# Performance work log

Hardware: AMD Instinct MI355X
Metric: run time of the kernel (lower is better)

The kernel has to match this reference:

```python
import jax, jax.numpy as jnp
import numpy as np

B, N, D = 8, 4096, 512
H, R = 8, 256
DEPTH = D // H


def setup_inputs() -> dict:
    key = jax.random.key(0)
    ks = jax.random.split(key, 8)
    g = lambda k, shape, fan: jax.random.normal(k, shape, jnp.float32) * np.sqrt(2.0 / fan)
    return {
        "x": jax.random.normal(ks[0], (B, N, D), jnp.float32),
        "wq": g(ks[1], (D, D), 2 * D),
        "wk": g(ks[2], (D, D), 2 * D),
        "wv": g(ks[3], (D, D), 2 * D),
        "E": g(ks[4], (H, N, R), N + R),
        "F": g(ks[5], (H, N, R), N + R),
        "w_dense": g(ks[6], (D, D), 2 * D),
        "b_dense": jnp.zeros((D,), jnp.float32),
    }


def reference(x, wq, wk, wv, E, F, w_dense, b_dense):
    b = x.shape[0]
    split = lambda t: t.reshape(b, N, H, DEPTH).transpose(0, 2, 1, 3)  # -> bhnd
    q = split(x @ wq)
    k = split(x @ wk)
    v = split(x @ wv)
    # low-rank Linformer projections of K and V along sequence dim
    k_proj = jnp.einsum('bhnd,hnr->bhrd', k, E)
    v_proj = jnp.einsum('bhnd,hnr->bhrd', v, F)
    scores = jnp.einsum('bhnd,bhrd->bhnr', q, k_proj) / jnp.sqrt(jnp.float32(DEPTH))
    attn = jax.nn.softmax(scores, axis=-1)
    out = jnp.einsum('bhnr,bhrd->bhnd', attn, v_proj)
    concat = out.transpose(0, 2, 1, 3).reshape(b, N, D)
    return concat @ w_dense + b_dense
```

## Files before the change

kernel.cpp:

```cpp
#include <hip/hip_runtime.h>


typedef __bf16 bf16;
typedef __attribute__((ext_vector_type(8))) __bf16 bf16x8;
typedef __attribute__((ext_vector_type(8))) unsigned short ushort8;
typedef __attribute__((ext_vector_type(4))) float floatx4;

#define MFMA16(a, b, c) __builtin_amdgcn_mfma_f32_16x16x32_bf16((a), (b), (c), 0, 0, 0)

static __device__ __forceinline__ unsigned short bf_bits(float f) {
  unsigned u = __builtin_bit_cast(unsigned, f);
  u += 0x7fffu + ((u >> 16) & 1u);
  return (unsigned short)(u >> 16);
}
static __device__ __forceinline__ bf16 f2bf(float f) {
  unsigned short s = bf_bits(f);
  return __builtin_bit_cast(bf16, s);
}
static __device__ __forceinline__ float bf2f(bf16 v) {
  unsigned u = (unsigned)__builtin_bit_cast(unsigned short, v) << 16;
  return __builtin_bit_cast(float, u);
}
static __device__ __forceinline__ void async_copy16(const void* g, void* l) {
  __builtin_amdgcn_global_load_lds((const __attribute__((address_space(1))) void*)g,
                                   (__attribute__((address_space(3))) void*)l, 16, 0, 0);
}

__global__ void cvt_bf16_kernel(const float* __restrict__ src, bf16* __restrict__ dst) {
  long i = ((long)blockIdx.x * 256 + threadIdx.x) * 8;
  float4 a = *(const float4*)(src + i);
  float4 b = *(const float4*)(src + i + 4);
  ushort8 o;
  o[0] = bf_bits(a.x); o[1] = bf_bits(a.y); o[2] = bf_bits(a.z); o[3] = bf_bits(a.w);
  o[4] = bf_bits(b.x); o[5] = bf_bits(b.y); o[6] = bf_bits(b.z); o[7] = bf_bits(b.w);
  *(ushort8*)(dst + i) = o;
}

__global__ void transpose_cvt_kernel(const float* __restrict__ src, bf16* __restrict__ dst,
                                     int K, int Nc, long src_z, long dst_z) {
  src += (long)blockIdx.z * src_z;
  dst += (long)blockIdx.z * dst_z;
  __shared__ float tile[32][33];
  const int k0 = blockIdx.x * 32, n0 = blockIdx.y * 32;
  const int tx = threadIdx.x, ty = threadIdx.y;
#pragma unroll
  for (int i = ty; i < 32; i += 8)
    tile[i][tx] = src[(long)(k0 + i) * Nc + n0 + tx];
  __syncthreads();
#pragma unroll
  for (int i = ty; i < 32; i += 8)
    dst[(long)(n0 + i) * K + k0 + tx] = f2bf(tile[tx][i]);
}

template <int MODE>
__global__ __launch_bounds__(256) void gemm128_kernel(
    const bf16* __restrict__ A, const bf16* __restrict__ Bt,
    bf16* __restrict__ oq, bf16* __restrict__ ok, bf16* __restrict__ ov,
    float* __restrict__ of, const float* __restrict__ bias) {
  __shared__ bf16 As[128][64];
  __shared__ bf16 Bs[128][64];
  const int m0 = blockIdx.y * 128, n0 = blockIdx.x * 128;
  const int t = threadIdx.x;
  const int w = t >> 6, l = t & 63, quad = l >> 4, lc = l & 15;
  const int wr = w >> 1, wc = w & 1;
  const int srow = w * 32 + (l >> 3);
  const int scol = (l & 7) * 8;
  const bf16* ga = A + (long)(m0 + srow) * 512 + scol;
  const bf16* gb = Bt + (long)(n0 + srow) * 512 + scol;
  floatx4 acc[4][4] = {};
  for (int k0 = 0; k0 < 512; k0 += 64) {
#pragma unroll
    for (int i = 0; i < 4; ++i) {
      async_copy16(ga + k0 + (long)i * 8 * 512, &As[w * 32 + i * 8][0]);
      async_copy16(gb + k0 + (long)i * 8 * 512, &Bs[w * 32 + i * 8][0]);
    }
    __syncthreads();
#pragma unroll
    for (int kk = 0; kk < 64; kk += 32) {
      bf16x8 af[4], bfr[4];
#pragma unroll
      for (int mt = 0; mt < 4; ++mt)
        af[mt] = *(const bf16x8*)&As[wr * 64 + mt * 16 + lc][kk + quad * 8];
#pragma unroll
      for (int nt = 0; nt < 4; ++nt)
        bfr[nt] = *(const bf16x8*)&Bs[wc * 64 + nt * 16 + lc][kk + quad * 8];
#pragma unroll
      for (int mt = 0; mt < 4; ++mt)
#pragma unroll
        for (int nt = 0; nt < 4; ++nt)
          acc[mt][nt] = MFMA16(af[mt], bfr[nt], acc[mt][nt]);
    }
    __syncthreads();
  }
  if (MODE == 0) {
    const int which = n0 >> 9, nb = n0 & 511;
    bf16* dst = which == 0 ? oq : (which == 1 ? ok : ov);
#pragma unroll
    for (int mt = 0; mt < 4; ++mt)
#pragma unroll
      for (int nt = 0; nt < 4; ++nt)
#pragma unroll
        for (int i = 0; i < 4; ++i) {
          int row = m0 + wr * 64 + mt * 16 + quad * 4 + i;
          int col = nb + wc * 64 + nt * 16 + lc;
          dst[(long)row * 512 + col] = f2bf(acc[mt][nt][i]);
        }
  } else {
#pragma unroll
    for (int mt = 0; mt < 4; ++mt)
#pragma unroll
      for (int nt = 0; nt < 4; ++nt)
#pragma unroll
        for (int i = 0; i < 4; ++i) {
          int row = m0 + wr * 64 + mt * 16 + quad * 4 + i;
          int col = n0 + wc * 64 + nt * 16 + lc;
          of[(long)row * 512 + col] = acc[mt][nt][i] + bias[col];
        }
  }
}

__global__ __launch_bounds__(256) void proj_kernel(
    const bf16* __restrict__ Et_g, const bf16* __restrict__ Ft_g,
    const bf16* __restrict__ kb, const bf16* __restrict__ vb,
    bf16* __restrict__ kp_part, bf16* __restrict__ vp_part) {
  const int z = blockIdx.z;
  const bf16* Big = z ? Ft_g : Et_g;
  const bf16* src = z ? vb : kb;
  bf16* out = z ? vp_part : kp_part;
  const int bh = blockIdx.y, b = bh >> 3, h = bh & 7;
  const int nbase = blockIdx.x * 1024;
  __shared__ bf16 Eb[256][64];
  __shared__ bf16 Kt[64][72];
  const int t = threadIdx.x;
  const int w = t >> 6, l = t & 63, quad = l >> 4, lc = l & 15;
  const int ecol = (l & 7) * 8;
  const bf16* gE = Big + ((long)h * 256 + w * 64 + (l >> 3)) * 4096 + nbase + ecol;
  const int sn = t >> 3, sq = t & 7;
  const bf16* gK = src + (long)(b * 4096 + nbase + sn) * 512 + h * 64 + sq * 8;
  floatx4 acc[4][4] = {};
  for (int ks = 0; ks < 16; ++ks) {
    bf16x8 kv0 = *(const bf16x8*)(gK + (long)(ks * 64) * 512);
    bf16x8 kv1 = *(const bf16x8*)(gK + (long)(ks * 64 + 32) * 512);
    __syncthreads();
#pragma unroll
    for (int i = 0; i < 8; ++i)
      async_copy16(gE + ks * 64 + (long)i * 8 * 4096, &Eb[w * 64 + i * 8][0]);
#pragma unroll
    for (int jj = 0; jj < 8; ++jj) Kt[sq * 8 + jj][sn ^ (sq * 8)] = kv0[jj];
#pragma unroll
    for (int jj = 0; jj < 8; ++jj) Kt[sq * 8 + jj][(32 + sn) ^ (sq * 8)] = kv1[jj];
    __syncthreads();
#pragma unroll
    for (int kk = 0; kk < 64; kk += 32) {
      bf16x8 af[4], bfr[4];
      if (z == 0) {
#pragma unroll
        for (int mt = 0; mt < 4; ++mt)
          af[mt] = *(const bf16x8*)&Eb[w * 64 + mt * 16 + lc][kk + quad * 8];
#pragma unroll
        for (int nt = 0; nt < 4; ++nt) {
          int d = nt * 16 + lc;
          bfr[nt] = *(const bf16x8*)&Kt[d][(kk + quad * 8) ^ ((d >> 3) << 3)];
        }
      } else {
#pragma unroll
        for (int mt = 0; mt < 4; ++mt) {
          int d = mt * 16 + lc;
          af[mt] = *(const bf16x8*)&Kt[d][(kk + quad * 8) ^ ((d >> 3) << 3)];
        }
#pragma unroll
        for (int nt = 0; nt < 4; ++nt)
          bfr[nt] = *(const bf16x8*)&Eb[w * 64 + nt * 16 + lc][kk + quad * 8];
      }
#pragma unroll
      for (int mt = 0; mt < 4; ++mt)
#pragma unroll
        for (int nt = 0; nt < 4; ++nt)
          acc[mt][nt] = MFMA16(af[mt], bfr[nt], acc[mt][nt]);
    }
  }
  bf16* obase = out + ((long)blockIdx.x * 64 + bh) * 16384;
  if (z == 0) {
#pragma unroll
    for (int mt = 0; mt < 4; ++mt)
#pragma unroll
      for (int nt = 0; nt < 4; ++nt)
#pragma unroll
        for (int i = 0; i < 4; ++i) {
          int r = w * 64 + mt * 16 + quad * 4 + i, d = nt * 16 + lc;
          obase[(long)r * 64 + d] = f2bf(acc[mt][nt][i]);
        }
  } else {
#pragma unroll
    for (int mt = 0; mt < 4; ++mt)
#pragma unroll
      for (int nt = 0; nt < 4; ++nt)
#pragma unroll
        for (int i = 0; i < 4; ++i) {
          int d = mt * 16 + quad * 4 + i, r = w * 64 + nt * 16 + lc;
          obase[(long)d * 256 + r] = f2bf(acc[mt][nt][i]);
        }
  }
}

__global__ void reduce_part_kernel(const bf16* __restrict__ part, bf16* __restrict__ out) {
  part += (long)blockIdx.z * 4194304;
  out += (long)blockIdx.z * 1048576;
  long i = ((long)blockIdx.x * 256 + threadIdx.x) * 8;
  bf16x8 a = *(const bf16x8*)(part + i);
  bf16x8 b = *(const bf16x8*)(part + 1048576 + i);
  bf16x8 c = *(const bf16x8*)(part + 2097152 + i);
  bf16x8 d = *(const bf16x8*)(part + 3145728 + i);
  bf16x8 o;
#pragma unroll
  for (int j = 0; j < 8; ++j)
    o[j] = f2bf(bf2f(a[j]) + bf2f(b[j]) + bf2f(c[j]) + bf2f(d[j]));
  *(bf16x8*)(out + i) = o;
}

__global__ __launch_bounds__(512) void attn_kernel(
    const bf16* __restrict__ qb, const bf16* __restrict__ kp_bf,
    const bf16* __restrict__ vpT_bf, bf16* __restrict__ ao) {
  const int bx = blockIdx.x, h = blockIdx.y, b = blockIdx.z;
  const int bh = b * 8 + h;
  __shared__ __align__(16) char smem_u[36864];
  __shared__ bf16 Pc[2][128][40];
  bf16(*kpl)[72] = (bf16(*)[72])smem_u;
  bf16(*vtl)[264] = (bf16(*)[264])smem_u;
  const int t = threadIdx.x;
  const int w = t >> 6, l = t & 63, quad = l >> 4, lc = l & 15;

  {
    const bf16* p = kp_bf + (long)bh * 16384;
#pragma unroll
    for (int j = 0; j < 4; ++j) {
      int e = (j * 512 + t) * 8;
      *(bf16x8*)&kpl[e >> 6][e & 63] = *(const bf16x8*)(p + e);
    }
  }
  __syncthreads();

  const long qrow = (long)(b * 4096 + bx * 128 + w * 16 + lc) * 512 + h * 64;
  floatx4 acc[16] = {};
#pragma unroll
  for (int kk = 0; kk < 64; kk += 32) {
    bf16x8 a = *(const bf16x8*)(qb + qrow + kk + quad * 8);
#pragma unroll
    for (int nt = 0; nt < 16; ++nt) {
      bf16x8 bfr = *(const bf16x8*)&kpl[nt * 16 + lc][kk + quad * 8];
      acc[nt] = MFMA16(a, bfr, acc[nt]);
    }
  }
  __syncthreads();

  {
    const bf16* p = vpT_bf + (long)bh * 16384;
#pragma unroll
    for (int j = 0; j < 4; ++j) {
      int e = (j * 512 + t) * 8;
      *(bf16x8*)&vtl[e >> 8][e & 255] = *(const bf16x8*)(p + e);
    }
  }

  float mx[4] = {-1e30f, -1e30f, -1e30f, -1e30f};
#pragma unroll
  for (int nt = 0; nt < 16; ++nt)
#pragma unroll
    for (int i = 0; i < 4; ++i) {
      acc[nt][i] *= 0.125f;
      mx[i] = fmaxf(mx[i], acc[nt][i]);
    }
#pragma unroll
  for (int m = 1; m <= 8; m <<= 1)
#pragma unroll
    for (int i = 0; i < 4; ++i) mx[i] = fmaxf(mx[i], __shfl_xor(mx[i], m, 64));
  float sm[4] = {0.f, 0.f, 0.f, 0.f};
#pragma unroll
  for (int nt = 0; nt < 16; ++nt)
#pragma unroll
    for (int i = 0; i < 4; ++i) {
      float p = __expf(acc[nt][i] - mx[i]);
      acc[nt][i] = p;
      sm[i] += p;
    }
#pragma unroll
  for (int m = 1; m <= 8; m <<= 1)
#pragma unroll
    for (int i = 0; i < 4; ++i) sm[i] += __shfl_xor(sm[i], m, 64);
  float inv[4];
#pragma unroll
  for (int i = 0; i < 4; ++i) inv[i] = 1.0f / sm[i];

  floatx4 acc2[4] = {};
  for (int rs = 0; rs < 8; ++rs) {
    const int buf = rs & 1;
#pragma unroll
    for (int u = 0; u < 2; ++u) {
      int nt = rs * 2 + u;
#pragma unroll
      for (int i = 0; i < 4; ++i)
        Pc[buf][w * 16 + quad * 4 + i][u * 16 + lc] = f2bf(acc[nt][i] * inv[i]);
    }
    __syncthreads();
    bf16x8 a2 = *(const bf16x8*)&Pc[buf][w * 16 + lc][quad * 8];
#pragma unroll
    for (int nt = 0; nt < 4; ++nt) {
      bf16x8 b2 = *(const bf16x8*)&vtl[nt * 16 + lc][rs * 32 + quad * 8];
      acc2[nt] = MFMA16(a2, b2, acc2[nt]);
    }
  }

#pragma unroll
  for (int nt = 0; nt < 4; ++nt)
#pragma unroll
    for (int i = 0; i < 4; ++i) {
      int row = bx * 128 + w * 16 + quad * 4 + i;
      int d = nt * 16 + lc;
      ao[(long)(b * 4096 + row) * 512 + h * 64 + d] = f2bf(acc2[nt][i]);
    }
}

extern "C" void kernel_launch(void* const* d_in, const int* in_sizes, int n_in,
                              void* d_out, int out_size, void* d_ws, size_t ws_size,
                              hipStream_t stream) {
  const float* x  = (const float*)d_in[0];
  const float* wq = (const float*)d_in[1];
  const float* wk = (const float*)d_in[2];
  const float* wv = (const float*)d_in[3];
  const float* E  = (const float*)d_in[4];
  const float* F  = (const float*)d_in[5];
  const float* wd = (const float*)d_in[6];
  const float* bd = (const float*)d_in[7];
  float* out = (float*)d_out;

  char* ws = (char*)d_ws;
  bf16* x_bf    = (bf16*)(ws + 0);
  bf16* q_bf    = (bf16*)(ws + 33554432l);
  bf16* k_bf    = (bf16*)(ws + 67108864l);
  bf16* v_bf    = (bf16*)(ws + 100663296l);
  bf16* Et_g    = (bf16*)(ws + 134217728l);
  bf16* Ft_g    = (bf16*)(ws + 150994944l);
  bf16* Wt      = (bf16*)(ws + 167772160l);
  bf16* wdT     = (bf16*)(ws + 169345024l);
  bf16* kp_part = (bf16*)(ws + 169869312l);
  bf16* vp_part = (bf16*)(ws + 178257920l);
  bf16* kp_bf   = (bf16*)(ws + 186646528l);
  bf16* vpT_bf  = (bf16*)(ws + 188743680l);
  bf16* attn_o  = x_bf;

  dim3 tb(32, 8);
  cvt_bf16_kernel<<<8192, 256, 0, stream>>>(x, x_bf);
  transpose_cvt_kernel<<<dim3(16, 16, 1), tb, 0, stream>>>(wq, Wt, 512, 512, 0, 0);
  transpose_cvt_kernel<<<dim3(16, 16, 1), tb, 0, stream>>>(wk, Wt + 512 * 512, 512, 512, 0, 0);
  transpose_cvt_kernel<<<dim3(16, 16, 1), tb, 0, stream>>>(wv, Wt + 2 * 512 * 512, 512, 512, 0, 0);
  transpose_cvt_kernel<<<dim3(16, 16, 1), tb, 0, stream>>>(wd, wdT, 512, 512, 0, 0);
  transpose_cvt_kernel<<<dim3(128, 8, 8), tb, 0, stream>>>(E, Et_g, 4096, 256,
                                                           4096l * 256, 4096l * 256);
  transpose_cvt_kernel<<<dim3(128, 8, 8), tb, 0, stream>>>(F, Ft_g, 4096, 256,
                                                           4096l * 256, 4096l * 256);

  gemm128_kernel<0><<<dim3(12, 256), 256, 0, stream>>>(x_bf, Wt, q_bf, k_bf, v_bf,
                                                       nullptr, nullptr);
  proj_kernel<<<dim3(4, 64, 2), 256, 0, stream>>>(Et_g, Ft_g, k_bf, v_bf, kp_part, vp_part);
  reduce_part_kernel<<<dim3(512, 1, 2), 256, 0, stream>>>(kp_part, kp_bf);
  attn_kernel<<<dim3(32, 8, 8), 512, 0, stream>>>(q_bf, kp_bf, vpT_bf, attn_o);
  gemm128_kernel<1><<<dim3(4, 256), 256, 0, stream>>>(attn_o, wdT, nullptr, nullptr, nullptr,
                                                      out, bd);
}
```

Measured before the change: 402.7 us.

## Fuse partial-sum reduction into attention and batch transpose launches with swizzled GEMM grid

Removes the separate reduce_part kernel by having the attention kernel sum the four split-K partials of the projected K and V while loading them into LDS. The six weight and E/F transpose launches are merged into two, and the GEMM grids become 1D with a remapping that spreads consecutive blocks across row groups, possibly for XCD/L2 locality. This saves launches and an extra global round trip. The cost is that every attention block (32 per head) now reads four partials instead of one reduced tensor.

```diff
diff --git a/kernel.cpp b/kernel.cpp
--- a/kernel.cpp
+++ b/kernel.cpp
@@ -36,20 +36,39 @@
   *(ushort8*)(dst + i) = o;
 }
 
-__global__ void transpose_cvt_kernel(const float* __restrict__ src, bf16* __restrict__ dst,
-                                     int K, int Nc, long src_z, long dst_z) {
-  src += (long)blockIdx.z * src_z;
-  dst += (long)blockIdx.z * dst_z;
+__global__ void transpose_w4_kernel(const float* __restrict__ wq, const float* __restrict__ wk,
+                                    const float* __restrict__ wv, const float* __restrict__ wd,
+                                    bf16* __restrict__ Wt, bf16* __restrict__ wdT) {
+  const int z = blockIdx.z;
+  const float* src = z == 0 ? wq : (z == 1 ? wk : (z == 2 ? wv : wd));
+  bf16* dst = z < 3 ? Wt + (long)z * 262144 : wdT;
   __shared__ float tile[32][33];
   const int k0 = blockIdx.x * 32, n0 = blockIdx.y * 32;
   const int tx = threadIdx.x, ty = threadIdx.y;
 #pragma unroll
   for (int i = ty; i < 32; i += 8)
-    tile[i][tx] = src[(long)(k0 + i) * Nc + n0 + tx];
+    tile[i][tx] = src[(long)(k0 + i) * 512 + n0 + tx];
   __syncthreads();
 #pragma unroll
   for (int i = ty; i < 32; i += 8)
-    dst[(long)(n0 + i) * K + k0 + tx] = f2bf(tile[tx][i]);
+    dst[(long)(n0 + i) * 512 + k0 + tx] = f2bf(tile[tx][i]);
+}
+
+__global__ void transpose_ef_kernel(const float* __restrict__ E, const float* __restrict__ F,
+                                    bf16* __restrict__ Et, bf16* __restrict__ Ft) {
+  const int z = blockIdx.z, h = z & 7;
+  const float* src = (z < 8 ? E : F) + (long)h * 4096 * 256;
+  bf16* dst = (z < 8 ? Et : Ft) + (long)h * 256 * 4096;
+  __shared__ float tile[32][33];
+  const int k0 = blockIdx.x * 32, n0 = blockIdx.y * 32;
+  const int tx = threadIdx.x, ty = threadIdx.y;
+#pragma unroll
+  for (int i = ty; i < 32; i += 8)
+    tile[i][tx] = src[(long)(k0 + i) * 256 + n0 + tx];
+  __syncthreads();
+#pragma unroll
+  for (int i = ty; i < 32; i += 8)
+    dst[(long)(n0 + i) * 4096 + k0 + tx] = f2bf(tile[tx][i]);
 }
 
 template <int MODE>
@@ -57,9 +76,12 @@
     const bf16* __restrict__ A, const bf16* __restrict__ Bt,
     bf16* __restrict__ oq, bf16* __restrict__ ok, bf16* __restrict__ ov,
     float* __restrict__ of, const float* __restrict__ bias) {
+  constexpr int NB = MODE == 0 ? 12 : 4;
+  const int lin = blockIdx.x;
+  const int p = lin & 7, q = lin >> 3;
+  const int m0 = (p * 32 + q / NB) * 128, n0 = (q % NB) * 128;
   __shared__ bf16 As[128][64];
   __shared__ bf16 Bs[128][64];
-  const int m0 = blockIdx.y * 128, n0 = blockIdx.x * 128;
   const int t = threadIdx.x;
   const int w = t >> 6, l = t & 63, quad = l >> 4, lc = l & 15;
   const int wr = w >> 1, wc = w & 1;
@@ -203,24 +225,9 @@
   }
 }
 
-__global__ void reduce_part_kernel(const bf16* __restrict__ part, bf16* __restrict__ out) {
-  part += (long)blockIdx.z * 4194304;
-  out += (long)blockIdx.z * 1048576;
-  long i = ((long)blockIdx.x * 256 + threadIdx.x) * 8;
-  bf16x8 a = *(const bf16x8*)(part + i);
-  bf16x8 b = *(const bf16x8*)(part + 1048576 + i);
-  bf16x8 c = *(const bf16x8*)(part + 2097152 + i);
-  bf16x8 d = *(const bf16x8*)(part + 3145728 + i);
-  bf16x8 o;
-#pragma unroll
-  for (int j = 0; j < 8; ++j)
-    o[j] = f2bf(bf2f(a[j]) + bf2f(b[j]) + bf2f(c[j]) + bf2f(d[j]));
-  *(bf16x8*)(out + i) = o;
-}
-
 __global__ __launch_bounds__(512) void attn_kernel(
-    const bf16* __restrict__ qb, const bf16* __restrict__ kp_bf,
-    const bf16* __restrict__ vpT_bf, bf16* __restrict__ ao) {
+    const bf16* __restrict__ qb, const bf16* __restrict__ kp_part,
+    const bf16* __restrict__ vp_part, bf16* __restrict__ ao) {
   const int bx = blockIdx.x, h = blockIdx.y, b = blockIdx.z;
   const int bh = b * 8 + h;
   __shared__ __align__(16) char smem_u[36864];
@@ -231,11 +238,20 @@
   const int w = t >> 6, l = t & 63, quad = l >> 4, lc = l & 15;
 
   {
-    const bf16* p = kp_bf + (long)bh * 16384;
+    const bf16* p = kp_part + (long)bh * 16384;
 #pragma unroll
     for (int j = 0; j < 4; ++j) {
-      int e = (j * 512 + t) * 8;
-      *(bf16x8*)&kpl[e >> 6][e & 63] = *(const bf16x8*)(p + e);
+      long e = (long)(j * 512 + t) * 8;
+      bf16x8 a = *(const bf16x8*)(p + e);
+      bf16x8 bb = *(const bf16x8*)(p + 1048576 + e);
+      bf16x8 c = *(const bf16x8*)(p + 2097152 + e);
+      bf16x8 d = *(const bf16x8*)(p + 3145728 + e);
+      bf16x8 o;
+#pragma unroll
+      for (int jj = 0; jj < 8; ++jj)
+        o[jj] = f2bf(bf2f(a[jj]) + bf2f(bb[jj]) + bf2f(c[jj]) + bf2f(d[jj]));
+      int e32 = j * 512 + t;
+      *(bf16x8*)&kpl[e32 >> 3][(e32 & 7) * 8] = o;
     }
   }
   __syncthreads();
@@ -254,11 +270,20 @@
   __syncthreads();
 
   {
-    const bf16* p = vpT_bf + (long)bh * 16384;
+    const bf16* p = vp_part + (long)bh * 16384;
 #pragma unroll
     for (int j = 0; j < 4; ++j) {
-      int e = (j * 512 + t) * 8;
-      *(bf16x8*)&vtl[e >> 8][e & 255] = *(const bf16x8*)(p + e);
+      long e = (long)(j * 512 + t) * 8;
+      bf16x8 a = *(const bf16x8*)(p + e);
+      bf16x8 bb = *(const bf16x8*)(p + 1048576 + e);
+      bf16x8 c = *(const bf16x8*)(p + 2097152 + e);
+      bf16x8 d = *(const bf16x8*)(p + 3145728 + e);
+      bf16x8 o;
+#pragma unroll
+      for (int jj = 0; jj < 8; ++jj)
+        o[jj] = f2bf(bf2f(a[jj]) + bf2f(bb[jj]) + bf2f(c[jj]) + bf2f(d[jj]));
+      int e32 = j * 512 + t;
+      *(bf16x8*)&vtl[e32 >> 5][(e32 & 31) * 8] = o;
     }
   }
 
@@ -279,9 +304,9 @@
   for (int nt = 0; nt < 16; ++nt)
 #pragma unroll
     for (int i = 0; i < 4; ++i) {
-      float p = __expf(acc[nt][i] - mx[i]);
-      acc[nt][i] = p;
-      sm[i] += p;
+      float pp = __expf(acc[nt][i] - mx[i]);
+      acc[nt][i] = pp;
+      sm[i] += pp;
     }
 #pragma unroll
   for (int m = 1; m <= 8; m <<= 1)
@@ -344,26 +369,15 @@
   bf16* wdT     = (bf16*)(ws + 169345024l);
   bf16* kp_part = (bf16*)(ws + 169869312l);
   bf16* vp_part = (bf16*)(ws + 178257920l);
-  bf16* kp_bf   = (bf16*)(ws + 186646528l);
-  bf16* vpT_bf  = (bf16*)(ws + 188743680l);
   bf16* attn_o  = x_bf;
 
   dim3 tb(32, 8);
   cvt_bf16_kernel<<<8192, 256, 0, stream>>>(x, x_bf);
-  transpose_cvt_kernel<<<dim3(16, 16, 1), tb, 0, stream>>>(wq, Wt, 512, 512, 0, 0);
-  transpose_cvt_kernel<<<dim3(16, 16, 1), tb, 0, stream>>>(wk, Wt + 512 * 512, 512, 512, 0, 0);
-  transpose_cvt_kernel<<<dim3(16, 16, 1), tb, 0, stream>>>(wv, Wt + 2 * 512 * 512, 512, 512, 0, 0);
-  transpose_cvt_kernel<<<dim3(16, 16, 1), tb, 0, stream>>>(wd, wdT, 512, 512, 0, 0);
-  transpose_cvt_kernel<<<dim3(128, 8, 8), tb, 0, stream>>>(E, Et_g, 4096, 256,
-                                                           4096l * 256, 4096l * 256);
-  transpose_cvt_kernel<<<dim3(128, 8, 8), tb, 0, stream>>>(F, Ft_g, 4096, 256,
-                                                           4096l * 256, 4096l * 256);
-
-  gemm128_kernel<0><<<dim3(12, 256), 256, 0, stream>>>(x_bf, Wt, q_bf, k_bf, v_bf,
-                                                       nullptr, nullptr);
+  transpose_w4_kernel<<<dim3(16, 16, 4), tb, 0, stream>>>(wq, wk, wv, wd, Wt, wdT);
+  transpose_ef_kernel<<<dim3(128, 8, 16), tb, 0, stream>>>(E, F, Et_g, Ft_g);
+
+  gemm128_kernel<0><<<3072, 256, 0, stream>>>(x_bf, Wt, q_bf, k_bf, v_bf, nullptr, nullptr);
   proj_kernel<<<dim3(4, 64, 2), 256, 0, stream>>>(Et_g, Ft_g, k_bf, v_bf, kp_part, vp_part);
-  reduce_part_kernel<<<dim3(512, 1, 2), 256, 0, stream>>>(kp_part, kp_bf);
-  attn_kernel<<<dim3(32, 8, 8), 512, 0, stream>>>(q_bf, kp_bf, vpT_bf, attn_o);
-  gemm128_kernel<1><<<dim3(4, 256), 256, 0, stream>>>(attn_o, wdT, nullptr, nullptr, nullptr,
-                                                      out, bd);
-}
+  attn_kernel<<<dim3(32, 8, 8), 512, 0, stream>>>(q_bf, kp_part, vp_part, attn_o);
+  gemm128_kernel<1><<<1024, 256, 0, stream>>>(attn_o, wdT, nullptr, nullptr, nullptr, out, bd);
+}
```

After: 390.4 us. -3.1%, faster.
